# Performance work log

Hardware: AMD Instinct MI355X
Metric: run time of the kernel (lower is better)

The kernel has to match this reference:

```python
import jax, jax.numpy as jnp
import numpy as np

EPS = 1e-5

def _ln(x, g, b):
    mu = jnp.mean(x, axis=-1, keepdims=True)
    var = jnp.mean(jnp.square(x - mu), axis=-1, keepdims=True)
    return (x - mu) * jax.lax.rsqrt(var + EPS) * g + b

def _lrelu(x):
    return jnp.where(x >= 0, x, 0.1 * x)  # LeakyReLU(0.1)

def _layer(x, w, b, g, be, act):
    # PointLinearLayer: Linear -> LayerNorm -> (optional) LeakyReLU(0.1)
    y = _ln(jnp.matmul(x, w) + b, g, be)
    return _lrelu(y) if act else y

def setup_inputs():
    key = jax.random.key(0)
    ks = jax.random.split(key, 16)
    B, Ns, Nd, K, Cin, Cout, PE, M = 1, 10000, 40000, 16, 128, 128, 32, 16
    w = lambda k, i, o: jax.random.normal(k, (i, o), jnp.float32) * 0.02
    z = lambda n: jnp.zeros((n,), jnp.float32)
    o = lambda n: jnp.ones((n,), jnp.float32)
    return {
        "sparse_xyz": jax.random.normal(ks[0], (B, Ns, 3), jnp.float32),
        "sparse_feats": jax.random.normal(ks[1], (B, Ns, Cin), jnp.float32),
        "nei_inds": jax.random.randint(ks[2], (B, Nd, K), 0, Ns),
        "sparse_xyz_norm": jax.random.normal(ks[3], (B, Ns, 3), jnp.float32),
        "dense_xyz": jax.random.normal(ks[4], (B, Nd, 3), jnp.float32),
        "dense_xyz_norm": jax.random.normal(ks[5], (B, Nd, 3), jnp.float32),
        "dense_feats": jax.random.normal(ks[6], (B, Nd, Cout), jnp.float32),
        # pe_convs WeightNet(3 -> 32, hidden=[32]): L0 3->32 LN+act, L1 32->32 LN
        "pe_w0": w(ks[7], 3, PE), "pe_b0": z(PE), "pe_g0": o(PE), "pe_be0": z(PE),
        "pe_w1": w(ks[8], PE, PE), "pe_b1": z(PE), "pe_g1": o(PE), "pe_be1": z(PE),
        # main WeightNet(3 -> 16, hidden=[16,16]): L0,L1 LN+act, L2 LN
        "wn_w0": w(ks[9], 3, M), "wn_b0": z(M), "wn_g0": o(M), "wn_be0": z(M),
        "wn_w1": w(ks[10], M, M), "wn_b1": z(M), "wn_g1": o(M), "wn_be1": z(M),
        "wn_w2": w(ks[11], M, M), "wn_b2": z(M), "wn_g2": o(M), "wn_be2": z(M),
        # final PointLinearLayer: (Cin+PE)*M -> Cout with LN + LeakyReLU(0.1)
        "lin_w": w(ks[12], (Cin + PE) * M, Cout), "lin_b": z(Cout),
        "lin_g": o(Cout), "lin_be": z(Cout),
    }

def reference(sparse_xyz, sparse_feats, nei_inds, sparse_xyz_norm, dense_xyz,
              dense_xyz_norm, dense_feats,
              pe_w0, pe_b0, pe_g0, pe_be0, pe_w1, pe_b1, pe_g1, pe_be1,
              wn_w0, wn_b0, wn_g0, wn_be0, wn_w1, wn_b1, wn_g1, wn_be1,
              wn_w2, wn_b2, wn_g2, wn_be2, lin_w, lin_b, lin_g, lin_be):
    gather = jax.vmap(lambda t, i: t[i])  # per-batch kNN gather
    loc = gather(sparse_xyz, nei_inds) - dense_xyz[:, :, None, :]   # B,Nd,K,3 relative coords (weightNetInput, USE_VI=False)
    g_feat = gather(sparse_feats, nei_inds)                          # B,Nd,K,Cin
    # positional-encoding WeightNet on relative coords (USE_PE)
    pe = _layer(loc, pe_w0, pe_b0, pe_g0, pe_be0, True)
    pe = _layer(pe, pe_w1, pe_b1, pe_g1, pe_be1, False)              # B,Nd,K,32
    feat = jnp.concatenate([g_feat, pe], axis=-1)                    # B,Nd,K,Cin+32
    # main WeightNet generates per-neighbor mixing weights
    wts = _layer(loc, wn_w0, wn_b0, wn_g0, wn_be0, True)
    wts = _layer(wts, wn_w1, wn_b1, wn_g1, wn_be1, True)
    wts = _layer(wts, wn_w2, wn_b2, wn_g2, wn_be2, False)            # B,Nd,K,16
    B, Nd = nei_inds.shape[:2]
    # matmul(feat^T, wts) over K, flatten channel x mid dims (C-major, matches torch .view)
    out = jnp.einsum('bnkc,bnkm->bncm', feat, wts).reshape(B, Nd, -1)
    out = _layer(out, lin_w, lin_b, lin_g, lin_be, True)             # B,Nd,Cout
    return out + dense_feats                                         # shortcut dense features
```

## Files before the change

kernel.cpp:

```cpp
#include <hip/hip_runtime.h>

#define NPB  16
#define KNN  16
#define CIN  128
#define CF   160
#define MM   16
#define PEC  32
#define COUT 128
#define KDIM 2560
#define LEPS 1e-5f

typedef __bf16 bf16x8 __attribute__((ext_vector_type(8)));
typedef float  f32x4  __attribute__((ext_vector_type(4)));
union U16x8 { uint4 u4; bf16x8 b; unsigned short us[8]; };

#define SW_PE_W0   0
#define SW_PE_B0   96
#define SW_PE_G0   128
#define SW_PE_BE0  160
#define SW_PE_W1   192
#define SW_PE_B1   1216
#define SW_PE_G1   1248
#define SW_PE_BE1  1280
#define SW_WN_W0   1312
#define SW_WN_B0   1360
#define SW_WN_G0   1376
#define SW_WN_BE0  1392
#define SW_WN_W1   1408
#define SW_WN_B1   1664
#define SW_WN_G1   1680
#define SW_WN_BE1  1696
#define SW_WN_W2   1712
#define SW_WN_B2   1968
#define SW_WN_G2   1984
#define SW_WN_BE2  2000
#define SW_TOTAL   2016

__device__ __forceinline__ float bf2f(unsigned short b){
  union { unsigned int u; float f; } x; x.u = ((unsigned int)b) << 16; return x.f;
}
__device__ __forceinline__ unsigned short f2bf(float f){
  union { float f; unsigned int u; } x; x.f = f;
  unsigned int r = (x.u + 0x7fffu + ((x.u >> 16) & 1u)) >> 16;
  return (unsigned short)r;
}
__device__ __forceinline__ unsigned short f2b(float f){
  union { __bf16 h; unsigned short u; } v; v.h = (__bf16)f; return v.u;
}
__device__ __forceinline__ float rsum16(float v){
  v += __shfl_xor(v, 8, 16);
  v += __shfl_xor(v, 4, 16);
  v += __shfl_xor(v, 2, 16);
  v += __shfl_xor(v, 1, 16);
  return v;
}
__device__ __forceinline__ float rsum8(float v){
  v += __shfl_xor(v, 4, 8);
  v += __shfl_xor(v, 2, 8);
  v += __shfl_xor(v, 1, 8);
  return v;
}
__device__ __forceinline__ float rsum32(float v){
  v += __shfl_xor(v, 16, 32);
  v += __shfl_xor(v, 8, 32);
  v += __shfl_xor(v, 4, 32);
  v += __shfl_xor(v, 2, 32);
  v += __shfl_xor(v, 1, 32);
  return v;
}
__device__ __forceinline__ float lrelu(float v){ return v >= 0.f ? v : 0.1f * v; }

template<int N>
__device__ __forceinline__ void ln_inlane(float* v, const float* g, const float* be, bool act){
  float mu = 0.f;
#pragma unroll
  for (int i = 0; i < N; ++i) mu += v[i];
  mu *= (1.f / N);
  float var = 0.f;
#pragma unroll
  for (int i = 0; i < N; ++i) { float d = v[i] - mu; var += d * d; }
  const float rs = rsqrtf(var * (1.f / N) + LEPS);
#pragma unroll
  for (int i = 0; i < N; ++i) {
    float y = (v[i] - mu) * rs * g[i] + be[i];
    v[i] = act ? lrelu(y) : y;
  }
}

__global__ __launch_bounds__(256)
void pct_prep(const float* __restrict__ lin_w, unsigned short* __restrict__ wpack,
              const float* __restrict__ sf, unsigned short* __restrict__ sfb16,
              const int n4)
{
  const int bid = blockIdx.x;
  if (bid < 160) {
    const int u    = bid * 256 + threadIdx.x;
    const int lane = u & 63;
    const int tt   = (u >> 6) & 7;
    const int s    = u >> 9;
    const int ipb  = s * 32 + ((lane >> 4) * 8);
    const int nn   = tt * 16 + (lane & 15);
    unsigned short v[8];
#pragma unroll
    for (int j = 0; j < 8; ++j) {
      const int ip  = ipb + j;
      const int r   = ip & 3;
      const int ctl = (ip >> 2) & 1;
      const int qq  = (ip >> 3) & 3;
      const int c16 = (ip >> 5) & 15;
      const int P   = ip >> 9;
      const int c   = P * 32 + ctl * 16 + c16;
      const int m   = qq * 4 + r;
      v[j] = f2bf(lin_w[(long)(c * MM + m) * COUT + nn]);
    }
    *(uint4*)(wpack + (long)u * 8) = *(uint4*)v;
  } else {
    const int i = (bid - 160) * 256 + threadIdx.x;
    if (i >= n4) return;
    const float4 v = ((const float4*)sf)[i];
    union { unsigned short us[4]; uint2 u; } r;
    r.us[0] = f2b(v.x); r.us[1] = f2b(v.y); r.us[2] = f2b(v.z); r.us[3] = f2b(v.w);
    ((uint2*)sfb16)[i] = r.u;
  }
}

__global__ __launch_bounds__(256)
void pct_einsum_mfma(
    const float* __restrict__ sparse_xyz,
    const int* __restrict__ nei_inds,
    const float* __restrict__ dense_xyz,
    const unsigned short* __restrict__ sfb16,
    const float* __restrict__ pe_w0, const float* __restrict__ pe_b0,
    const float* __restrict__ pe_g0, const float* __restrict__ pe_be0,
    const float* __restrict__ pe_w1, const float* __restrict__ pe_b1,
    const float* __restrict__ pe_g1, const float* __restrict__ pe_be1,
    const float* __restrict__ wn_w0, const float* __restrict__ wn_b0,
    const float* __restrict__ wn_g0, const float* __restrict__ wn_be0,
    const float* __restrict__ wn_w1, const float* __restrict__ wn_b1,
    const float* __restrict__ wn_g1, const float* __restrict__ wn_be1,
    const float* __restrict__ wn_w2, const float* __restrict__ wn_b2,
    const float* __restrict__ wn_g2, const float* __restrict__ wn_be2,
    unsigned short* __restrict__ apack)
{
  __shared__ __align__(16) float zeroblk[128];
  __shared__ __align__(16) unsigned short wtsf[16 * 256];
  __shared__ __align__(16) unsigned short pef[16 * 512];
  __shared__ __align__(16) union SU {
    float sw[SW_TOTAL];
    char  stage[4 * 2 * 4096];
  } su;
  float* sw = su.sw;

  const int t     = threadIdx.x;
  const int nbase = blockIdx.x * NPB;

  if (t < 128) zeroblk[t] = 0.f;
  for (int i = t; i < 96;   i += 256) sw[SW_PE_W0 + i] = pe_w0[i];
  for (int i = t; i < 32;   i += 256) {
    sw[SW_PE_B0 + i] = pe_b0[i];  sw[SW_PE_G0 + i] = pe_g0[i];  sw[SW_PE_BE0 + i] = pe_be0[i];
    sw[SW_PE_B1 + i] = pe_b1[i];  sw[SW_PE_G1 + i] = pe_g1[i];  sw[SW_PE_BE1 + i] = pe_be1[i];
  }
  for (int i = t; i < 1024; i += 256) sw[SW_PE_W1 + i] = pe_w1[i];
  for (int i = t; i < 48;   i += 256) sw[SW_WN_W0 + i] = wn_w0[i];
  for (int i = t; i < 16;   i += 256) {
    sw[SW_WN_B0 + i] = wn_b0[i];  sw[SW_WN_G0 + i] = wn_g0[i];  sw[SW_WN_BE0 + i] = wn_be0[i];
    sw[SW_WN_B1 + i] = wn_b1[i];  sw[SW_WN_G1 + i] = wn_g1[i];  sw[SW_WN_BE1 + i] = wn_be1[i];
    sw[SW_WN_B2 + i] = wn_b2[i];  sw[SW_WN_G2 + i] = wn_g2[i];  sw[SW_WN_BE2 + i] = wn_be2[i];
  }
  for (int i = t; i < 256;  i += 256) { sw[SW_WN_W1 + i] = wn_w1[i]; sw[SW_WN_W2 + i] = wn_w2[i]; }
  __syncthreads();

  {
    const int p  = t >> 4;
    const int kk = t & 15;
    const int n  = nbase + p;
    const int idx = nei_inds[n * KNN + kk];
    const float x0 = sparse_xyz[idx*3+0] - dense_xyz[n*3+0];
    const float x1 = sparse_xyz[idx*3+1] - dense_xyz[n*3+1];
    const float x2 = sparse_xyz[idx*3+2] - dense_xyz[n*3+2];

    float h[32];
#pragma unroll
    for (int c = 0; c < 32; ++c)
      h[c] = x0*sw[SW_PE_W0+c] + x1*sw[SW_PE_W0+32+c] + x2*sw[SW_PE_W0+64+c] + sw[SW_PE_B0+c];
    ln_inlane<32>(h, &sw[SW_PE_G0], &sw[SW_PE_BE0], true);

    float z[32];
#pragma unroll
    for (int c = 0; c < 32; ++c) z[c] = sw[SW_PE_B1 + c];
#pragma unroll 4
    for (int j = 0; j < 32; ++j) {
      const float hj = h[j];
#pragma unroll
      for (int c = 0; c < 32; ++c) z[c] += hj * sw[SW_PE_W1 + j*32 + c];
    }
    ln_inlane<32>(z, &sw[SW_PE_G1], &sw[SW_PE_BE1], false);
    {
      union { unsigned short us[32]; uint4 u4[4]; } zb;
#pragma unroll
      for (int c = 0; c < 32; ++c) zb.us[c] = f2b(z[c]);
      unsigned short* pp_ = pef + p*512 + kk*32;
#pragma unroll
      for (int j = 0; j < 4; ++j) *(uint4*)(pp_ + j*8) = zb.u4[j];
    }

    float w[16];
#pragma unroll
    for (int m = 0; m < 16; ++m)
      w[m] = x0*sw[SW_WN_W0+m] + x1*sw[SW_WN_W0+16+m] + x2*sw[SW_WN_W0+32+m] + sw[SW_WN_B0+m];
    ln_inlane<16>(w, &sw[SW_WN_G0], &sw[SW_WN_BE0], true);

    float z2[16];
#pragma unroll
    for (int m = 0; m < 16; ++m) z2[m] = sw[SW_WN_B1 + m];
#pragma unroll 4
    for (int j = 0; j < 16; ++j) {
      const float wj = w[j];
#pragma unroll
      for (int m = 0; m < 16; ++m) z2[m] += wj * sw[SW_WN_W1 + j*16 + m];
    }
    ln_inlane<16>(z2, &sw[SW_WN_G1], &sw[SW_WN_BE1], true);

#pragma unroll
    for (int m = 0; m < 16; ++m) w[m] = sw[SW_WN_B2 + m];
#pragma unroll 4
    for (int j = 0; j < 16; ++j) {
      const float wj = z2[j];
#pragma unroll
      for (int m = 0; m < 16; ++m) w[m] += wj * sw[SW_WN_W2 + j*16 + m];
    }
    ln_inlane<16>(w, &sw[SW_WN_G2], &sw[SW_WN_BE2], false);
    {
      unsigned short* wf = wtsf + p*256 + ((kk >> 3) << 7) + (kk & 7);
#pragma unroll
      for (int m = 0; m < 16; ++m) wf[m*8] = f2b(w[m]);
    }
  }
  __syncthreads();

  const int lane = t & 63;
  const int wave = t >> 6;
  const int q    = lane >> 4;
  const int mq   = lane & 15;
  char* stw = su.stage + wave * 8192;

  int idxall[4][4];
#pragma unroll
  for (int i = 0; i < 4; ++i)
#pragma unroll
    for (int t4 = 0; t4 < 4; ++t4)
      idxall[i][t4] = nei_inds[(nbase + wave*4 + i) * KNN + t4*4 + q];

#pragma unroll
  for (int t4 = 0; t4 < 4; ++t4)
    __builtin_amdgcn_global_load_lds(
        (const void*)(sfb16 + (size_t)idxall[0][t4] * CIN + mq * 8),
        (void*)(stw + t4 * 1024), 16, 0, 0);

  f32x4 accs[10];
#pragma unroll
  for (int i = 0; i < 4; ++i) {
    const int p = wave * 4 + i;
    const size_t n = (size_t)(nbase + p);

    if (i < 3) {
#pragma unroll
      for (int t4 = 0; t4 < 4; ++t4)
        __builtin_amdgcn_global_load_lds(
            (const void*)(sfb16 + (size_t)idxall[i+1][t4] * CIN + mq * 8),
            (void*)(stw + ((i+1) & 1) * 4096 + t4 * 1024), 16, 0, 0);
    }
    if (i == 0)      asm volatile("s_waitcnt vmcnt(4)" ::: "memory");
    else if (i == 1) asm volatile("s_waitcnt vmcnt(9)" ::: "memory");
    else if (i == 2) asm volatile("s_waitcnt vmcnt(9)" ::: "memory");
    else             asm volatile("s_waitcnt vmcnt(5)" ::: "memory");
    __builtin_amdgcn_sched_barrier(0);

    U16x8 af;
    {
      const unsigned short* ap_ = (lane < 32)
          ? wtsf + p * 256 + lane * 8
          : (const unsigned short*)zeroblk + (lane - 32) * 8;
      af.u4 = *(const uint4*)ap_;
    }
#pragma unroll
    for (int ct = 0; ct < 10; ++ct) accs[ct] = (f32x4){0.f, 0.f, 0.f, 0.f};

    const unsigned short* sb = (const unsigned short*)(stw + (i & 1) * 4096)
                               + (q & 1) * 1024 + mq;
#pragma unroll
    for (int ct = 0; ct < 8; ++ct) {
      U16x8 bf_;
#pragma unroll
      for (int j = 0; j < 8; ++j) bf_.us[j] = sb[j * CIN + ct * 16];
      accs[ct] = __builtin_amdgcn_mfma_f32_16x16x32_bf16(af.b, bf_.b, accs[ct], 0, 0, 0);
    }
    const unsigned short* pb = pef + p * 512 + (q & 1) * 256 + mq;
#pragma unroll
    for (int ct = 0; ct < 2; ++ct) {
      U16x8 bf_;
#pragma unroll
      for (int j = 0; j < 8; ++j) bf_.us[j] = pb[j * 32 + ct * 16];
      accs[8 + ct] = __builtin_amdgcn_mfma_f32_16x16x32_bf16(af.b, bf_.b, accs[8 + ct], 0, 0, 0);
    }

    unsigned short* ap = apack + n * KDIM + mq * 32 + q * 8;
#pragma unroll
    for (int P = 0; P < 5; ++P) {
      union { unsigned short us[8]; uint4 u4; } o;
#pragma unroll
      for (int r = 0; r < 4; ++r) {
        o.us[r]     = f2b(accs[2*P    ][r]);
        o.us[4 + r] = f2b(accs[2*P + 1][r]);
      }
      *(uint4*)(ap + P * 512) = o.u4;
    }
  }
}

__global__ __launch_bounds__(256, 4)
void pct_gemm32(
    const unsigned short* __restrict__ apack,
    const unsigned short* __restrict__ wpack,
    const float* __restrict__ lin_b, const float* __restrict__ lin_g,
    const float* __restrict__ lin_be, const float* __restrict__ dense_feats,
    float* __restrict__ out)
{
  __shared__ float out_s[32][132];

  const int t    = threadIdx.x;
  const int lane = t & 63;
  const int wave = t >> 6;
  const int n0   = blockIdx.x * 32;

  const unsigned short* arow0 = apack + (long)(n0 + (lane & 15)) * KDIM + ((lane >> 4) * 8);
  const unsigned short* arow1 = arow0 + (long)16 * KDIM;
  const unsigned short* wp0   = wpack + ((long)(wave*2) * 64 + lane) * 8;

  f32x4 acc00 = {0.f,0.f,0.f,0.f}, acc01 = {0.f,0.f,0.f,0.f};
  f32x4 acc10 = {0.f,0.f,0.f,0.f}, acc11 = {0.f,0.f,0.f,0.f};

  U16x8 a0[4], a1[4], b0[4], b1[4];
#pragma unroll
  for (int d = 0; d < 4; ++d) {
    a0[d].u4 = *(const uint4*)(arow0 + d*32);
    a1[d].u4 = *(const uint4*)(arow1 + d*32);
    b0[d].u4 = *(const uint4*)(wp0 + (long)d*4096);
    b1[d].u4 = *(const uint4*)(wp0 + (long)d*4096 + 512);
  }

#pragma unroll 4
  for (int s = 0; s < 76; ++s) {
    const int d = s & 3;
    __builtin_amdgcn_sched_barrier(0);
    acc00 = __builtin_amdgcn_mfma_f32_16x16x32_bf16(a0[d].b, b0[d].b, acc00, 0, 0, 0);
    acc01 = __builtin_amdgcn_mfma_f32_16x16x32_bf16(a0[d].b, b1[d].b, acc01, 0, 0, 0);
    acc10 = __builtin_amdgcn_mfma_f32_16x16x32_bf16(a1[d].b, b0[d].b, acc10, 0, 0, 0);
    acc11 = __builtin_amdgcn_mfma_f32_16x16x32_bf16(a1[d].b, b1[d].b, acc11, 0, 0, 0);
    __builtin_amdgcn_sched_barrier(0);
    a0[d].u4 = *(const uint4*)(arow0 + (s+4)*32);
    a1[d].u4 = *(const uint4*)(arow1 + (s+4)*32);
    b0[d].u4 = *(const uint4*)(wp0 + (long)(s+4)*4096);
    b1[d].u4 = *(const uint4*)(wp0 + (long)(s+4)*4096 + 512);
  }
#pragma unroll
  for (int s = 76; s < 80; ++s) {
    const int d = s & 3;
    __builtin_amdgcn_sched_barrier(0);
    acc00 = __builtin_amdgcn_mfma_f32_16x16x32_bf16(a0[d].b, b0[d].b, acc00, 0, 0, 0);
    acc01 = __builtin_amdgcn_mfma_f32_16x16x32_bf16(a0[d].b, b1[d].b, acc01, 0, 0, 0);
    acc10 = __builtin_amdgcn_mfma_f32_16x16x32_bf16(a1[d].b, b0[d].b, acc10, 0, 0, 0);
    acc11 = __builtin_amdgcn_mfma_f32_16x16x32_bf16(a1[d].b, b1[d].b, acc11, 0, 0, 0);
  }
  __builtin_amdgcn_sched_barrier(0);

  {
    const int quad = lane >> 4;
    const int colb = wave*32 + (lane & 15);
#pragma unroll
    for (int r = 0; r < 4; ++r) {
      out_s[     quad*4 + r][colb     ] = acc00[r];
      out_s[     quad*4 + r][colb + 16] = acc01[r];
      out_s[16 + quad*4 + r][colb     ] = acc10[r];
      out_s[16 + quad*4 + r][colb + 16] = acc11[r];
    }
  }
  __syncthreads();

  {
    const int p  = t >> 3;
    const int l8 = t & 7;
    const int n  = n0 + p;
    float v[16];
#pragma unroll
    for (int i = 0; i < 4; ++i) {
      const int cb = (i*8 + l8) * 4;
      const float4 r  = *(const float4*)(&out_s[p][cb]);
      const float4 bb = *(const float4*)(lin_b + cb);
      v[i*4+0] = r.x + bb.x; v[i*4+1] = r.y + bb.y;
      v[i*4+2] = r.z + bb.z; v[i*4+3] = r.w + bb.w;
    }
    float sum = 0.f;
#pragma unroll
    for (int i = 0; i < 16; ++i) sum += v[i];
    const float mu = rsum8(sum) * (1.f/128.f);
    float qs = 0.f;
#pragma unroll
    for (int i = 0; i < 16; ++i) { float d = v[i] - mu; qs += d*d; }
    const float rs = rsqrtf(rsum8(qs) * (1.f/128.f) + LEPS);
#pragma unroll
    for (int i = 0; i < 4; ++i) {
      const int cb = (i*8 + l8) * 4;
      const float4 g  = *(const float4*)(lin_g  + cb);
      const float4 be = *(const float4*)(lin_be + cb);
      const float4 df = *(const float4*)(dense_feats + (long)n*COUT + cb);
      float4 y;
      y.x = lrelu((v[i*4+0]-mu)*rs*g.x + be.x) + df.x;
      y.y = lrelu((v[i*4+1]-mu)*rs*g.y + be.y) + df.y;
      y.z = lrelu((v[i*4+2]-mu)*rs*g.z + be.z) + df.z;
      y.w = lrelu((v[i*4+3]-mu)*rs*g.w + be.w) + df.w;
      *(float4*)(out + (long)n*COUT + cb) = y;
    }
  }
}

__global__ __launch_bounds__(256)
void pct_fused(
    const float* __restrict__ sparse_xyz,
    const float* __restrict__ sparse_feats,
    const int* __restrict__ nei_inds,
    const float* __restrict__ dense_xyz,
    const float* __restrict__ dense_feats,
    const float* __restrict__ pe_w0, const float* __restrict__ pe_b0,
    const float* __restrict__ pe_g0, const float* __restrict__ pe_be0,
    const float* __restrict__ pe_w1, const float* __restrict__ pe_b1,
    const float* __restrict__ pe_g1, const float* __restrict__ pe_be1,
    const float* __restrict__ wn_w0, const float* __restrict__ wn_b0,
    const float* __restrict__ wn_g0, const float* __restrict__ wn_be0,
    const float* __restrict__ wn_w1, const float* __restrict__ wn_b1,
    const float* __restrict__ wn_g1, const float* __restrict__ wn_be1,
    const float* __restrict__ wn_w2, const float* __restrict__ wn_b2,
    const float* __restrict__ wn_g2, const float* __restrict__ wn_be2,
    const float* __restrict__ lin_w, const float* __restrict__ lin_b,
    const float* __restrict__ lin_g, const float* __restrict__ lin_be,
    float* __restrict__ out)
{
  __shared__ __align__(16) unsigned short feat_s[KNN][CF];
  __shared__ float wts_s[KNN][MM];
  __shared__ float loc_s[KNN][3];
  __shared__ int   nei_s[KNN];
  __shared__ __align__(16) unsigned short out_tile[CF*MM][8];

  const int t  = threadIdx.x;
  const int n0 = blockIdx.x * 8;
  const int k  = t >> 4;
  const int l  = t & 15;

#pragma unroll 1
  for (int p = 0; p < 8; ++p) {
    const int n = n0 + p;
    if (t < KNN) {
      int idx = nei_inds[n*KNN + t];
      nei_s[t] = idx;
      loc_s[t][0] = sparse_xyz[idx*3+0] - dense_xyz[n*3+0];
      loc_s[t][1] = sparse_xyz[idx*3+1] - dense_xyz[n*3+1];
      loc_s[t][2] = sparse_xyz[idx*3+2] - dense_xyz[n*3+2];
    }
    __syncthreads();
    {
      const int gk = t >> 4;
      const int c8 = (t & 15) * 8;
      const float* src = sparse_feats + (long)nei_s[gk]*CIN + c8;
      const float4 va = *(const float4*)(src);
      const float4 vb = *(const float4*)(src + 4);
      unsigned short* dst = &feat_s[gk][c8];
      dst[0] = f2bf(va.x); dst[1] = f2bf(va.y); dst[2] = f2bf(va.z); dst[3] = f2bf(va.w);
      dst[4] = f2bf(vb.x); dst[5] = f2bf(vb.y); dst[6] = f2bf(vb.z); dst[7] = f2bf(vb.w);
    }
    const float x0 = loc_s[k][0], x1 = loc_s[k][1], x2 = loc_s[k][2];
    const int c0 = l, c1 = l + 16;
    float ha = x0*pe_w0[0*PEC+c0] + x1*pe_w0[1*PEC+c0] + x2*pe_w0[2*PEC+c0] + pe_b0[c0];
    float hb = x0*pe_w0[0*PEC+c1] + x1*pe_w0[1*PEC+c1] + x2*pe_w0[2*PEC+c1] + pe_b0[c1];
    {
      float mu = rsum16(ha + hb) * (1.f/32.f);
      float da = ha - mu, db = hb - mu;
      float q  = rsum16(da*da + db*db);
      float rs = rsqrtf(q*(1.f/32.f) + LEPS);
      ha = lrelu(da*rs*pe_g0[c0] + pe_be0[c0]);
      hb = lrelu(db*rs*pe_g0[c1] + pe_be0[c1]);
    }
    float za = pe_b1[c0], zb = pe_b1[c1];
#pragma unroll
    for (int j = 0; j < 16; ++j) {
      float va = __shfl(ha, j, 16);
      float vb = __shfl(hb, j, 16);
      za += va * pe_w1[j*PEC + c0] + vb * pe_w1[(j+16)*PEC + c0];
      zb += va * pe_w1[j*PEC + c1] + vb * pe_w1[(j+16)*PEC + c1];
    }
    {
      float mu = rsum16(za + zb) * (1.f/32.f);
      float da = za - mu, db = zb - mu;
      float q  = rsum16(da*da + db*db);
      float rs = rsqrtf(q*(1.f/32.f) + LEPS);
      feat_s[k][CIN + c0] = f2bf(da*rs*pe_g1[c0] + pe_be1[c0]);
      feat_s[k][CIN + c1] = f2bf(db*rs*pe_g1[c1] + pe_be1[c1]);
    }
    float w0v = x0*wn_w0[0*MM+l] + x1*wn_w0[1*MM+l] + x2*wn_w0[2*MM+l] + wn_b0[l];
    {
      float mu = rsum16(w0v) * (1.f/16.f);
      float d  = w0v - mu;
      float rs = rsqrtf(rsum16(d*d)*(1.f/16.f) + LEPS);
      w0v = lrelu(d*rs*wn_g0[l] + wn_be0[l]);
    }
    float w1v = wn_b1[l];
#pragma unroll
    for (int j = 0; j < 16; ++j)
      w1v += __shfl(w0v, j, 16) * wn_w1[j*MM + l];
    {
      float mu = rsum16(w1v) * (1.f/16.f);
      float d  = w1v - mu;
      float rs = rsqrtf(rsum16(d*d)*(1.f/16.f) + LEPS);
      w1v = lrelu(d*rs*wn_g1[l] + wn_be1[l]);
    }
    float w2v = wn_b2[l];
#pragma unroll
    for (int j = 0; j < 16; ++j)
      w2v += __shfl(w1v, j, 16) * wn_w2[j*MM + l];
    {
      float mu = rsum16(w2v) * (1.f/16.f);
      float d  = w2v - mu;
      float rs = rsqrtf(rsum16(d*d)*(1.f/16.f) + LEPS);
      w2v = d*rs*wn_g2[l] + wn_be2[l];
    }
    wts_s[k][l] = w2v;
    __syncthreads();
    {
      const int m = t & 15;
      const int g = t >> 4;
      float wv[KNN];
#pragma unroll
      for (int kk = 0; kk < KNN; ++kk) wv[kk] = wts_s[kk][m];
#pragma unroll
      for (int j = 0; j < 10; ++j) {
        const int c = g*10 + j;
        float acc = 0.f;
#pragma unroll
        for (int kk = 0; kk < KNN; ++kk)
          acc += bf2f(feat_s[kk][c]) * wv[kk];
        out_tile[c*MM + m][p] = f2bf(acc);
      }
    }
    __syncthreads();
  }
  {
    const int h  = t >> 6;
    const int o0 = (t & 63) * 2;
    float acc0[8], acc1[8];
#pragma unroll
    for (int p = 0; p < 8; ++p) { acc0[p] = 0.f; acc1[p] = 0.f; }
    const int i0 = h * 640;
    for (int i = i0; i < i0 + 640; ++i) {
      const float2 wv = *(const float2*)(lin_w + (long)i*COUT + o0);
      const float wa = wv.x;
      const float wc = wv.y;
      const uint4 r = *(const uint4*)(&out_tile[i][0]);
      const float f0 = bf2f((unsigned short)(r.x & 0xffffu));
      const float f1 = bf2f((unsigned short)(r.x >> 16));
      const float g2 = bf2f((unsigned short)(r.y & 0xffffu));
      const float g3 = bf2f((unsigned short)(r.y >> 16));
      const float g4 = bf2f((unsigned short)(r.z & 0xffffu));
      const float g5 = bf2f((unsigned short)(r.z >> 16));
      const float g6 = bf2f((unsigned short)(r.w & 0xffffu));
      const float g7 = bf2f((unsigned short)(r.w >> 16));
      acc0[0] += f0*wa; acc1[0] += f0*wc;
      acc0[1] += f1*wa; acc1[1] += f1*wc;
      acc0[2] += g2*wa; acc1[2] += g2*wc;
      acc0[3] += g3*wa; acc1[3] += g3*wc;
      acc0[4] += g4*wa; acc1[4] += g4*wc;
      acc0[5] += g5*wa; acc1[5] += g5*wc;
      acc0[6] += g6*wa; acc1[6] += g6*wc;
      acc0[7] += g7*wa; acc1[7] += g7*wc;
    }
    __syncthreads();
    float* red = (float*)&out_tile[0][0];
#pragma unroll
    for (int p = 0; p < 8; ++p) {
      red[((h*8 + p) << 7) + o0    ] = acc0[p];
      red[((h*8 + p) << 7) + o0 + 1] = acc1[p];
    }
    __syncthreads();
    const int p2 = t >> 5, l2 = t & 31;
    const int n  = n0 + p2;
    float v[4];
#pragma unroll
    for (int j = 0; j < 4; ++j) {
      const int o = l2 + (j << 5);
      float sv = red[((0*8 + p2) << 7) + o] + red[((1*8 + p2) << 7) + o]
               + red[((2*8 + p2) << 7) + o] + red[((3*8 + p2) << 7) + o];
      v[j] = sv + lin_b[o];
    }
    float mu = rsum32(v[0] + v[1] + v[2] + v[3]) * (1.f/128.f);
    float q = 0.f;
#pragma unroll
    for (int j = 0; j < 4; ++j) { float d = v[j] - mu; q += d*d; }
    float rs = rsqrtf(rsum32(q) * (1.f/128.f) + LEPS);
#pragma unroll
    for (int j = 0; j < 4; ++j) {
      const int o = l2 + (j << 5);
      float y = (v[j] - mu) * rs * lin_g[o] + lin_be[o];
      y = lrelu(y);
      y += dense_feats[n*COUT + o];
      out[n*COUT + o] = y;
    }
  }
}

extern "C" void kernel_launch(void* const* d_in, const int* in_sizes, int n_in,
                              void* d_out, int out_size, void* d_ws, size_t ws_size,
                              hipStream_t stream) {
  const int Nd = in_sizes[2] / KNN;
  const int Ns = in_sizes[1] / CIN;
  const size_t a_bytes = (size_t)Nd * KDIM * 2;
  const size_t w_bytes = (size_t)KDIM * COUT * 2;
  const size_t f_bytes = (size_t)Ns * CIN * 2;
  const bool use_split = (ws_size >= a_bytes + w_bytes + f_bytes)
                         && (Nd % 32 == 0) && ((Ns * CIN) % 4 == 0);

  if (use_split) {
    unsigned short* apack = (unsigned short*)d_ws;
    unsigned short* wpack = (unsigned short*)((char*)d_ws + a_bytes);
    unsigned short* sfb16 = (unsigned short*)((char*)d_ws + a_bytes + w_bytes);

    const int n4 = Ns * CIN / 4;
    pct_prep<<<dim3(160 + (n4 + 255)/256), dim3(256), 0, stream>>>(
      (const float*)d_in[27], wpack, (const float*)d_in[1], sfb16, n4);

    pct_einsum_mfma<<<dim3(Nd / NPB), dim3(256), 0, stream>>>(
      (const float*)d_in[0],  (const int*)d_in[2],  (const float*)d_in[4],
      sfb16,
      (const float*)d_in[7],  (const float*)d_in[8],  (const float*)d_in[9],  (const float*)d_in[10],
      (const float*)d_in[11], (const float*)d_in[12], (const float*)d_in[13], (const float*)d_in[14],
      (const float*)d_in[15], (const float*)d_in[16], (const float*)d_in[17], (const float*)d_in[18],
      (const float*)d_in[19], (const float*)d_in[20], (const float*)d_in[21], (const float*)d_in[22],
      (const float*)d_in[23], (const float*)d_in[24], (const float*)d_in[25], (const float*)d_in[26],
      apack);

    pct_gemm32<<<dim3(Nd / 32), dim3(256), 0, stream>>>(
      apack, wpack,
      (const float*)d_in[28], (const float*)d_in[29], (const float*)d_in[30],
      (const float*)d_in[6], (float*)d_out);
  } else {
    pct_fused<<<dim3(Nd / 8), dim3(256), 0, stream>>>(
      (const float*)d_in[0],  (const float*)d_in[1],  (const int*)d_in[2],
      (const float*)d_in[4],  (const float*)d_in[6],
      (const float*)d_in[7],  (const float*)d_in[8],  (const float*)d_in[9],  (const float*)d_in[10],
      (const float*)d_in[11], (const float*)d_in[12], (const float*)d_in[13], (const float*)d_in[14],
      (const float*)d_in[15], (const float*)d_in[16], (const float*)d_in[17], (const float*)d_in[18],
      (const float*)d_in[19], (const float*)d_in[20], (const float*)d_in[21], (const float*)d_in[22],
      (const float*)d_in[23], (const float*)d_in[24], (const float*)d_in[25], (const float*)d_in[26],
      (const float*)d_in[27], (const float*)d_in[28], (const float*)d_in[29], (const float*)d_in[30],
      (float*)d_out);
  }
}
```

Measured before the change: 341.2 us.

## Split weight-net computation from gather-einsum and pipeline neighbor gathers via LDS

Moves the per-neighbor PE and WeightNet MLPs into a separate kernel that writes bf16 MFMA-ready fragments to workspace. A new einsum kernel then only gathers features through double-buffered global_load_lds with explicit vmcnt waits and runs the MFMAs. It requests higher occupancy through launch bounds. The aim is to stop the register-heavy MLP code from limiting occupancy and latency hiding in the gather/MFMA kernel. The cost is an extra launch plus a workspace write and read of the fragments, and the path only runs when the workspace is large enough.

Result: no change. 344.0 us (+0.8%).

```diff
diff --git a/kernel.cpp b/kernel.cpp
--- a/kernel.cpp
+++ b/kernel.cpp
@@ -8,6 +8,7 @@
 #define PEC  32
 #define COUT 128
 #define KDIM 2560
+#define FRE  768
 #define LEPS 1e-5f
 
 typedef __bf16 bf16x8 __attribute__((ext_vector_type(8)));
@@ -122,6 +123,221 @@
     r.us[0] = f2b(v.x); r.us[1] = f2b(v.y); r.us[2] = f2b(v.z); r.us[3] = f2b(v.w);
     ((uint2*)sfb16)[i] = r.u;
   }
+}
+
+__global__ __launch_bounds__(256)
+void pct_nets(
+    const float* __restrict__ sparse_xyz,
+    const int* __restrict__ nei_inds,
+    const float* __restrict__ dense_xyz,
+    const float* __restrict__ pe_w0, const float* __restrict__ pe_b0,
+    const float* __restrict__ pe_g0, const float* __restrict__ pe_be0,
+    const float* __restrict__ pe_w1, const float* __restrict__ pe_b1,
+    const float* __restrict__ pe_g1, const float* __restrict__ pe_be1,
+    const float* __restrict__ wn_w0, const float* __restrict__ wn_b0,
+    const float* __restrict__ wn_g0, const float* __restrict__ wn_be0,
+    const float* __restrict__ wn_w1, const float* __restrict__ wn_b1,
+    const float* __restrict__ wn_g1, const float* __restrict__ wn_be1,
+    const float* __restrict__ wn_w2, const float* __restrict__ wn_b2,
+    const float* __restrict__ wn_g2, const float* __restrict__ wn_be2,
+    unsigned short* __restrict__ frag_ws)
+{
+  __shared__ float sw[SW_TOTAL];
+  __shared__ __align__(16) unsigned short wtsf[16 * 256];
+  __shared__ __align__(16) unsigned short pef[16 * 512];
+
+  const int t     = threadIdx.x;
+  const int nbase = blockIdx.x * NPB;
+
+  for (int i = t; i < 96;   i += 256) sw[SW_PE_W0 + i] = pe_w0[i];
+  for (int i = t; i < 32;   i += 256) {
+    sw[SW_PE_B0 + i] = pe_b0[i];  sw[SW_PE_G0 + i] = pe_g0[i];  sw[SW_PE_BE0 + i] = pe_be0[i];
+    sw[SW_PE_B1 + i] = pe_b1[i];  sw[SW_PE_G1 + i] = pe_g1[i];  sw[SW_PE_BE1 + i] = pe_be1[i];
+  }
+  for (int i = t; i < 1024; i += 256) sw[SW_PE_W1 + i] = pe_w1[i];
+  for (int i = t; i < 48;   i += 256) sw[SW_WN_W0 + i] = wn_w0[i];
+  for (int i = t; i < 16;   i += 256) {
+    sw[SW_WN_B0 + i] = wn_b0[i];  sw[SW_WN_G0 + i] = wn_g0[i];  sw[SW_WN_BE0 + i] = wn_be0[i];
+    sw[SW_WN_B1 + i] = wn_b1[i];  sw[SW_WN_G1 + i] = wn_g1[i];  sw[SW_WN_BE1 + i] = wn_be1[i];
+    sw[SW_WN_B2 + i] = wn_b2[i];  sw[SW_WN_G2 + i] = wn_g2[i];  sw[SW_WN_BE2 + i] = wn_be2[i];
+  }
+  for (int i = t; i < 256;  i += 256) { sw[SW_WN_W1 + i] = wn_w1[i]; sw[SW_WN_W2 + i] = wn_w2[i]; }
+  __syncthreads();
+
+  {
+    const int p  = t >> 4;
+    const int kk = t & 15;
+    const int n  = nbase + p;
+    const int idx = nei_inds[n * KNN + kk];
+    const float x0 = sparse_xyz[idx*3+0] - dense_xyz[n*3+0];
+    const float x1 = sparse_xyz[idx*3+1] - dense_xyz[n*3+1];
+    const float x2 = sparse_xyz[idx*3+2] - dense_xyz[n*3+2];
+
+    float h[32];
+#pragma unroll
+    for (int c = 0; c < 32; ++c)
+      h[c] = x0*sw[SW_PE_W0+c] + x1*sw[SW_PE_W0+32+c] + x2*sw[SW_PE_W0+64+c] + sw[SW_PE_B0+c];
+    ln_inlane<32>(h, &sw[SW_PE_G0], &sw[SW_PE_BE0], true);
+
+    float z[32];
+#pragma unroll
+    for (int c = 0; c < 32; ++c) z[c] = sw[SW_PE_B1 + c];
+#pragma unroll 4
+    for (int j = 0; j < 32; ++j) {
+      const float hj = h[j];
+#pragma unroll
+      for (int c = 0; c < 32; ++c) z[c] += hj * sw[SW_PE_W1 + j*32 + c];
+    }
+    ln_inlane<32>(z, &sw[SW_PE_G1], &sw[SW_PE_BE1], false);
+    {
+      union { unsigned short us[32]; uint4 u4[4]; } zb;
+#pragma unroll
+      for (int c = 0; c < 32; ++c) zb.us[c] = f2b(z[c]);
+      unsigned short* pp_ = pef + p*512 + kk*32;
+#pragma unroll
+      for (int j = 0; j < 4; ++j) *(uint4*)(pp_ + j*8) = zb.u4[j];
+    }
+
+    float w[16];
+#pragma unroll
+    for (int m = 0; m < 16; ++m)
+      w[m] = x0*sw[SW_WN_W0+m] + x1*sw[SW_WN_W0+16+m] + x2*sw[SW_WN_W0+32+m] + sw[SW_WN_B0+m];
+    ln_inlane<16>(w, &sw[SW_WN_G0], &sw[SW_WN_BE0], true);
+
+    float z2[16];
+#pragma unroll
+    for (int m = 0; m < 16; ++m) z2[m] = sw[SW_WN_B1 + m];
+#pragma unroll 4
+    for (int j = 0; j < 16; ++j) {
+      const float wj = w[j];
+#pragma unroll
+      for (int m = 0; m < 16; ++m) z2[m] += wj * sw[SW_WN_W1 + j*16 + m];
+    }
+    ln_inlane<16>(z2, &sw[SW_WN_G1], &sw[SW_WN_BE1], true);
+
+#pragma unroll
+    for (int m = 0; m < 16; ++m) w[m] = sw[SW_WN_B2 + m];
+#pragma unroll 4
+    for (int j = 0; j < 16; ++j) {
+      const float wj = z2[j];
+#pragma unroll
+      for (int m = 0; m < 16; ++m) w[m] += wj * sw[SW_WN_W2 + j*16 + m];
+    }
+    ln_inlane<16>(w, &sw[SW_WN_G2], &sw[SW_WN_BE2], false);
+    {
+      unsigned short* wf = wtsf + p*256 + ((kk >> 3) << 7) + (kk & 7);
+#pragma unroll
+      for (int m = 0; m < 16; ++m) wf[m*8] = f2b(w[m]);
+    }
+  }
+
+  {
+    const int lane = t & 63;
+    const int wave = t >> 6;
+    const int l2   = lane & 31;
+    const int ct2  = lane >> 5;
+#pragma unroll
+    for (int i = 0; i < 4; ++i) {
+      const int p = wave*4 + i;
+      unsigned short* fw = frag_ws + (size_t)(nbase + p) * FRE;
+      if (lane < 32) {
+        const uint4 a = *(const uint4*)(wtsf + p*256 + lane*8);
+        *(uint4*)(fw + lane*8) = a;
+      }
+      union { unsigned short us[8]; uint4 u4; } o;
+#pragma unroll
+      for (int j = 0; j < 8; ++j)
+        o.us[j] = pef[p*512 + ((l2 >> 4)*8 + j)*32 + ct2*16 + (l2 & 15)];
+      *(uint4*)(fw + 256 + ct2*256 + l2*8) = o.u4;
+    }
+  }
+}
+
+__global__ __launch_bounds__(256, 4)
+void pct_einsum2(
+    const int* __restrict__ nei_inds,
+    const unsigned short* __restrict__ sfb16,
+    const unsigned short* __restrict__ frag_ws,
+    unsigned short* __restrict__ apack)
+{
+  __shared__ __align__(16) char stage[4 * 2 * 4096];
+
+  const int t     = threadIdx.x;
+  const int nbase = blockIdx.x * NPB;
+  const int lane  = t & 63;
+  const int wave  = t >> 6;
+  const int q     = lane >> 4;
+  const int mq    = lane & 15;
+  char* stw = stage + wave * 8192;
+
+  int idxall[4][4];
+#pragma unroll
+  for (int i = 0; i < 4; ++i)
+#pragma unroll
+    for (int t4 = 0; t4 < 4; ++t4)
+      idxall[i][t4] = nei_inds[(nbase + wave*4 + i) * KNN + t4*4 + q];
+
+  U16x8 af[2], pe0[2], pe1[2];
+  const uint4 zero4 = {0u, 0u, 0u, 0u};
+
+#define LOADF(i_, b_) do {                                                    \
+    const unsigned short* fw_ = frag_ws + (size_t)(nbase + wave*4 + (i_)) * FRE; \
+    af[b_].u4  = (lane < 32) ? *(const uint4*)(fw_ + lane*8) : zero4;          \
+    pe0[b_].u4 = *(const uint4*)(fw_ + 256 + (lane & 31)*8);                   \
+    pe1[b_].u4 = *(const uint4*)(fw_ + 512 + (lane & 31)*8);                   \
+  } while (0)
+
+#define GLDS(i_, b_) do {                                                     \
+    _Pragma("unroll")                                                         \
+    for (int t4 = 0; t4 < 4; ++t4)                                            \
+      __builtin_amdgcn_global_load_lds(                                       \
+          (const void*)(sfb16 + (size_t)idxall[i_][t4] * CIN + mq * 8),       \
+          (void*)(stw + (b_) * 4096 + t4 * 1024), 16, 0, 0);                  \
+  } while (0)
+
+  LOADF(0, 0);
+  GLDS(0, 0);
+
+  f32x4 accs[10];
+#pragma unroll
+  for (int i = 0; i < 4; ++i) {
+    const size_t n = (size_t)(nbase + wave*4 + i);
+
+    if (i < 3) { LOADF(i+1, (i+1)&1); GLDS(i+1, (i+1)&1); }
+    if (i == 0)      asm volatile("s_waitcnt vmcnt(7)"  ::: "memory");
+    else if (i == 3) asm volatile("s_waitcnt vmcnt(5)"  ::: "memory");
+    else             asm volatile("s_waitcnt vmcnt(12)" ::: "memory");
+    __builtin_amdgcn_sched_barrier(0);
+
+#pragma unroll
+    for (int ct = 0; ct < 10; ++ct) accs[ct] = (f32x4){0.f, 0.f, 0.f, 0.f};
+
+    const unsigned short* sb = (const unsigned short*)(stw + (i & 1) * 4096)
+                               + (q & 1) * 1024 + mq;
+#pragma unroll
+    for (int ct = 0; ct < 8; ++ct) {
+      U16x8 bf_;
+#pragma unroll
+      for (int j = 0; j < 8; ++j) bf_.us[j] = sb[j * CIN + ct * 16];
+      accs[ct] = __builtin_amdgcn_mfma_f32_16x16x32_bf16(af[i&1].b, bf_.b, accs[ct], 0, 0, 0);
+    }
+    accs[8] = __builtin_amdgcn_mfma_f32_16x16x32_bf16(af[i&1].b, pe0[i&1].b, accs[8], 0, 0, 0);
+    accs[9] = __builtin_amdgcn_mfma_f32_16x16x32_bf16(af[i&1].b, pe1[i&1].b, accs[9], 0, 0, 0);
+
+    unsigned short* ap = apack + n * KDIM + mq * 32 + q * 8;
+#pragma unroll
+    for (int P = 0; P < 5; ++P) {
+      union { unsigned short us[8]; uint4 u4; } o;
+#pragma unroll
+      for (int r = 0; r < 4; ++r) {
+        o.us[r]     = f2b(accs[2*P    ][r]);
+        o.us[4 + r] = f2b(accs[2*P + 1][r]);
+      }
+      *(uint4*)(ap + P * 512) = o.u4;
+    }
+  }
+#undef LOADF
+#undef GLDS
 }
 
 __global__ __launch_bounds__(256)
@@ -620,30 +836,47 @@
                               hipStream_t stream) {
   const int Nd = in_sizes[2] / KNN;
   const int Ns = in_sizes[1] / CIN;
-  const size_t a_bytes = (size_t)Nd * KDIM * 2;
-  const size_t w_bytes = (size_t)KDIM * COUT * 2;
-  const size_t f_bytes = (size_t)Ns * CIN * 2;
-  const bool use_split = (ws_size >= a_bytes + w_bytes + f_bytes)
-                         && (Nd % 32 == 0) && ((Ns * CIN) % 4 == 0);
-
-  if (use_split) {
+  const size_t a_bytes  = (size_t)Nd * KDIM * 2;
+  const size_t w_bytes  = (size_t)KDIM * COUT * 2;
+  const size_t f_bytes  = (size_t)Ns * CIN * 2;
+  const size_t fr_bytes = (size_t)Nd * FRE * 2;
+  const bool base_ok  = (Nd % 32 == 0) && ((Ns * CIN) % 4 == 0);
+  const bool use_split2 = base_ok && (ws_size >= a_bytes + w_bytes + f_bytes + fr_bytes);
+  const bool use_split1 = base_ok && (ws_size >= a_bytes + w_bytes + f_bytes);
+
+  if (use_split1) {
     unsigned short* apack = (unsigned short*)d_ws;
     unsigned short* wpack = (unsigned short*)((char*)d_ws + a_bytes);
     unsigned short* sfb16 = (unsigned short*)((char*)d_ws + a_bytes + w_bytes);
+    unsigned short* fragw = (unsigned short*)((char*)d_ws + a_bytes + w_bytes + f_bytes);
 
     const int n4 = Ns * CIN / 4;
     pct_prep<<<dim3(160 + (n4 + 255)/256), dim3(256), 0, stream>>>(
       (const float*)d_in[27], wpack, (const float*)d_in[1], sfb16, n4);
 
-    pct_einsum_mfma<<<dim3(Nd / NPB), dim3(256), 0, stream>>>(
-      (const float*)d_in[0],  (const int*)d_in[2],  (const float*)d_in[4],
-      sfb16,
-      (const float*)d_in[7],  (const float*)d_in[8],  (const float*)d_in[9],  (const float*)d_in[10],
-      (const float*)d_in[11], (const float*)d_in[12], (const float*)d_in[13], (const float*)d_in[14],
-      (const float*)d_in[15], (const float*)d_in[16], (const float*)d_in[17], (const float*)d_in[18],
-      (const float*)d_in[19], (const float*)d_in[20], (const float*)d_in[21], (const float*)d_in[22],
-      (const float*)d_in[23], (const float*)d_in[24], (const float*)d_in[25], (const float*)d_in[26],
-      apack);
+    if (use_split2) {
+      pct_nets<<<dim3(Nd / NPB), dim3(256), 0, stream>>>(
+        (const float*)d_in[0],  (const int*)d_in[2],  (const float*)d_in[4],
+        (const float*)d_in[7],  (const float*)d_in[8],  (const float*)d_in[9],  (const float*)d_in[10],
+        (const float*)d_in[11], (const float*)d_in[12], (const float*)d_in[13], (const float*)d_in[14],
+        (const float*)d_in[15], (const float*)d_in[16], (const float*)d_in[17], (const float*)d_in[18],
+        (const float*)d_in[19], (const float*)d_in[20], (const float*)d_in[21], (const float*)d_in[22],
+        (const float*)d_in[23], (const float*)d_in[24], (const float*)d_in[25], (const float*)d_in[26],
+        fragw);
+
+      pct_einsum2<<<dim3(Nd / NPB), dim3(256), 0, stream>>>(
+        (const int*)d_in[2], sfb16, fragw, apack);
+    } else {
+      pct_einsum_mfma<<<dim3(Nd / NPB), dim3(256), 0, stream>>>(
+        (const float*)d_in[0],  (const int*)d_in[2],  (const float*)d_in[4],
+        sfb16,
+        (const float*)d_in[7],  (const float*)d_in[8],  (const float*)d_in[9],  (const float*)d_in[10],
+        (const float*)d_in[11], (const float*)d_in[12], (const float*)d_in[13], (const float*)d_in[14],
+        (const float*)d_in[15], (const float*)d_in[16], (const float*)d_in[17], (const float*)d_in[18],
+        (const float*)d_in[19], (const float*)d_in[20], (const float*)d_in[21], (const float*)d_in[22],
+        (const float*)d_in[23], (const float*)d_in[24], (const float*)d_in[25], (const float*)d_in[26],
+        apack);
+    }
 
     pct_gemm32<<<dim3(Nd / 32), dim3(256), 0, stream>>>(
       apack, wpack,
```

## Split weight-net and gather-einsum into separate kernels staged through workspace

Applied to the files above, without the earlier changes.

The fused einsum kernel is split in two. `pct_nets` computes the PE and WeightNet MLPs and writes the bf16 weight and PE fragments into the apack rows as scratch. A new `pct_einsum2` kernel, launched with occupancy bound 4, reloads those fragments from global memory alongside the double-buffered global_load_lds gather of sparse features, then writes the einsum result over the same rows. The aim is to separate the register- and LDS-heavy MLP stage from the latency-bound gather and MFMA stage so the latter can run at higher occupancy. The cost is an extra kernel launch and an extra global write and read of the intermediate fragments.

After: 361.5 us. 5.9% more time.

```diff
diff --git a/kernel.cpp b/kernel.cpp
--- a/kernel.cpp
+++ b/kernel.cpp
@@ -125,11 +125,10 @@
 }
 
 __global__ __launch_bounds__(256)
-void pct_einsum_mfma(
+void pct_nets(
     const float* __restrict__ sparse_xyz,
     const int* __restrict__ nei_inds,
     const float* __restrict__ dense_xyz,
-    const unsigned short* __restrict__ sfb16,
     const float* __restrict__ pe_w0, const float* __restrict__ pe_b0,
     const float* __restrict__ pe_g0, const float* __restrict__ pe_be0,
     const float* __restrict__ pe_w1, const float* __restrict__ pe_b1,
@@ -142,19 +141,13 @@
     const float* __restrict__ wn_g2, const float* __restrict__ wn_be2,
     unsigned short* __restrict__ apack)
 {
-  __shared__ __align__(16) float zeroblk[128];
+  __shared__ float sw[SW_TOTAL];
   __shared__ __align__(16) unsigned short wtsf[16 * 256];
   __shared__ __align__(16) unsigned short pef[16 * 512];
-  __shared__ __align__(16) union SU {
-    float sw[SW_TOTAL];
-    char  stage[4 * 2 * 4096];
-  } su;
-  float* sw = su.sw;
 
   const int t     = threadIdx.x;
   const int nbase = blockIdx.x * NPB;
 
-  if (t < 128) zeroblk[t] = 0.f;
   for (int i = t; i < 96;   i += 256) sw[SW_PE_W0 + i] = pe_w0[i];
   for (int i = t; i < 32;   i += 256) {
     sw[SW_PE_B0 + i] = pe_b0[i];  sw[SW_PE_G0 + i] = pe_g0[i];  sw[SW_PE_BE0 + i] = pe_be0[i];
@@ -236,13 +229,44 @@
       for (int m = 0; m < 16; ++m) wf[m*8] = f2b(w[m]);
     }
   }
-  __syncthreads();
-
-  const int lane = t & 63;
-  const int wave = t >> 6;
-  const int q    = lane >> 4;
-  const int mq   = lane & 15;
-  char* stw = su.stage + wave * 8192;
+
+  {
+    const int lane = t & 63;
+    const int wave = t >> 6;
+    const int l2   = lane & 31;
+    const int ct2  = lane >> 5;
+#pragma unroll
+    for (int i = 0; i < 4; ++i) {
+      const int p = wave*4 + i;
+      unsigned short* fw = apack + (size_t)(nbase + p) * KDIM;
+      if (lane < 32) {
+        const uint4 a = *(const uint4*)(wtsf + p*256 + lane*8);
+        *(uint4*)(fw + lane*8) = a;
+      }
+      union { unsigned short us[8]; uint4 u4; } o;
+#pragma unroll
+      for (int j = 0; j < 8; ++j)
+        o.us[j] = pef[p*512 + ((l2 >> 4)*8 + j)*32 + ct2*16 + (l2 & 15)];
+      *(uint4*)(fw + 256 + ct2*256 + l2*8) = o.u4;
+    }
+  }
+}
+
+__global__ __launch_bounds__(256, 4)
+void pct_einsum2(
+    const int* __restrict__ nei_inds,
+    const unsigned short* __restrict__ sfb16,
+    unsigned short* __restrict__ apack)
+{
+  __shared__ __align__(16) char stage[4 * 2 * 4096];
+
+  const int t     = threadIdx.x;
+  const int nbase = blockIdx.x * NPB;
+  const int lane  = t & 63;
+  const int wave  = t >> 6;
+  const int q     = lane >> 4;
+  const int mq    = lane & 15;
+  char* stw = stage + wave * 8192;
 
   int idxall[4][4];
 #pragma unroll
@@ -251,38 +275,39 @@
     for (int t4 = 0; t4 < 4; ++t4)
       idxall[i][t4] = nei_inds[(nbase + wave*4 + i) * KNN + t4*4 + q];
 
-#pragma unroll
-  for (int t4 = 0; t4 < 4; ++t4)
-    __builtin_amdgcn_global_load_lds(
-        (const void*)(sfb16 + (size_t)idxall[0][t4] * CIN + mq * 8),
-        (void*)(stw + t4 * 1024), 16, 0, 0);
+  U16x8 af[2], pe0[2], pe1[2];
+  const uint4 zero4 = {0u, 0u, 0u, 0u};
+
+#define LOADF(i_, b_) do {                                                     \
+    const unsigned short* fw_ = apack + (size_t)(nbase + wave*4 + (i_)) * KDIM; \
+    af[b_].u4  = (lane < 32) ? *(const uint4*)(fw_ + lane*8) : zero4;          \
+    pe0[b_].u4 = *(const uint4*)(fw_ + 256 + (lane & 31)*8);                   \
+    pe1[b_].u4 = *(const uint4*)(fw_ + 512 + (lane & 31)*8);                   \
+  } while (0)
+
+#define GLDS(i_, b_) do {                                                     \
+    _Pragma("unroll")                                                         \
+    for (int t4 = 0; t4 < 4; ++t4)                                            \
+      __builtin_amdgcn_global_load_lds(                                       \
+          (const void*)(sfb16 + (size_t)idxall[i_][t4] * CIN + mq * 8),       \
+          (void*)(stw + (b_) * 4096 + t4 * 1024), 16, 0, 0);                  \
+  } while (0)
+
+  LOADF(0, 0);
+  GLDS(0, 0);
 
   f32x4 accs[10];
 #pragma unroll
   for (int i = 0; i < 4; ++i) {
-    const int p = wave * 4 + i;
-    const size_t n = (size_t)(nbase + p);
-
-    if (i < 3) {
-#pragma unroll
-      for (int t4 = 0; t4 < 4; ++t4)
-        __builtin_amdgcn_global_load_lds(
-            (const void*)(sfb16 + (size_t)idxall[i+1][t4] * CIN + mq * 8),
-            (void*)(stw + ((i+1) & 1) * 4096 + t4 * 1024), 16, 0, 0);
-    }
-    if (i == 0)      asm volatile("s_waitcnt vmcnt(4)" ::: "memory");
-    else if (i == 1) asm volatile("s_waitcnt vmcnt(9)" ::: "memory");
-    else if (i == 2) asm volatile("s_waitcnt vmcnt(9)" ::: "memory");
-    else             asm volatile("s_waitcnt vmcnt(5)" ::: "memory");
+    const size_t n = (size_t)(nbase + wave*4 + i);
+
     __builtin_amdgcn_sched_barrier(0);
-
-    U16x8 af;
-    {
-      const unsigned short* ap_ = (lane < 32)
-          ? wtsf + p * 256 + lane * 8
-          : (const unsigned short*)zeroblk + (lane - 32) * 8;
-      af.u4 = *(const uint4*)ap_;
-    }
+    if (i < 3) { LOADF(i+1, (i+1)&1); GLDS(i+1, (i+1)&1); }
+    if (i == 0)      asm volatile("s_waitcnt vmcnt(7)"  ::: "memory");
+    else if (i == 3) asm volatile("s_waitcnt vmcnt(5)"  ::: "memory");
+    else             asm volatile("s_waitcnt vmcnt(12)" ::: "memory");
+    __builtin_amdgcn_sched_barrier(0);
+
 #pragma unroll
     for (int ct = 0; ct < 10; ++ct) accs[ct] = (f32x4){0.f, 0.f, 0.f, 0.f};
 
@@ -293,16 +318,10 @@
       U16x8 bf_;
 #pragma unroll
       for (int j = 0; j < 8; ++j) bf_.us[j] = sb[j * CIN + ct * 16];
-      accs[ct] = __builtin_amdgcn_mfma_f32_16x16x32_bf16(af.b, bf_.b, accs[ct], 0, 0, 0);
-    }
-    const unsigned short* pb = pef + p * 512 + (q & 1) * 256 + mq;
-#pragma unroll
-    for (int ct = 0; ct < 2; ++ct) {
-      U16x8 bf_;
-#pragma unroll
-      for (int j = 0; j < 8; ++j) bf_.us[j] = pb[j * 32 + ct * 16];
-      accs[8 + ct] = __builtin_amdgcn_mfma_f32_16x16x32_bf16(af.b, bf_.b, accs[8 + ct], 0, 0, 0);
-    }
+      accs[ct] = __builtin_amdgcn_mfma_f32_16x16x32_bf16(af[i&1].b, bf_.b, accs[ct], 0, 0, 0);
+    }
+    accs[8] = __builtin_amdgcn_mfma_f32_16x16x32_bf16(af[i&1].b, pe0[i&1].b, accs[8], 0, 0, 0);
+    accs[9] = __builtin_amdgcn_mfma_f32_16x16x32_bf16(af[i&1].b, pe1[i&1].b, accs[9], 0, 0, 0);
 
     unsigned short* ap = apack + n * KDIM + mq * 32 + q * 8;
 #pragma unroll
@@ -316,6 +335,8 @@
       *(uint4*)(ap + P * 512) = o.u4;
     }
   }
+#undef LOADF
+#undef GLDS
 }
 
 __global__ __launch_bounds__(256, 4)
@@ -620,9 +641,9 @@
                               hipStream_t stream) {
   const int Nd = in_sizes[2] / KNN;
   const int Ns = in_sizes[1] / CIN;
-  const size_t a_bytes = (size_t)Nd * KDIM * 2;
-  const size_t w_bytes = (size_t)KDIM * COUT * 2;
-  const size_t f_bytes = (size_t)Ns * CIN * 2;
+  const size_t a_bytes  = (size_t)Nd * KDIM * 2;
+  const size_t w_bytes  = (size_t)KDIM * COUT * 2;
+  const size_t f_bytes  = (size_t)Ns * CIN * 2;
   const bool use_split = (ws_size >= a_bytes + w_bytes + f_bytes)
                          && (Nd % 32 == 0) && ((Ns * CIN) % 4 == 0);
 
@@ -635,15 +656,17 @@
     pct_prep<<<dim3(160 + (n4 + 255)/256), dim3(256), 0, stream>>>(
       (const float*)d_in[27], wpack, (const float*)d_in[1], sfb16, n4);
 
-    pct_einsum_mfma<<<dim3(Nd / NPB), dim3(256), 0, stream>>>(
+    pct_nets<<<dim3(Nd / NPB), dim3(256), 0, stream>>>(
       (const float*)d_in[0],  (const int*)d_in[2],  (const float*)d_in[4],
-      sfb16,
       (const float*)d_in[7],  (const float*)d_in[8],  (const float*)d_in[9],  (const float*)d_in[10],
       (const float*)d_in[11], (const float*)d_in[12], (const float*)d_in[13], (const float*)d_in[14],
       (const float*)d_in[15], (const float*)d_in[16], (const float*)d_in[17], (const float*)d_in[18],
       (const float*)d_in[19], (const float*)d_in[20], (const float*)d_in[21], (const float*)d_in[22],
       (const float*)d_in[23], (const float*)d_in[24], (const float*)d_in[25], (const float*)d_in[26],
       apack);
+
+    pct_einsum2<<<dim3(Nd / NPB), dim3(256), 0, stream>>>(
+      (const int*)d_in[2], sfb16, apack);
 
     pct_gemm32<<<dim3(Nd / 32), dim3(256), 0, stream>>>(
       apack, wpack,
```
